# Kernel optimization log

Measured on AMD Instinct MI355X. Metric: run time of the kernel, lower is better.

## Reference

```python
import jax, jax.numpy as jnp
import numpy as np

N, D, E = 50000, 128, 800000
BN_EPS = 1e-5


def _gcn(x, W, b, row, col, val):
    # dropout with p=0.0 is identity; h = x @ W; out = adj @ h + b (COO SpMM)
    h = x @ W                                    # [N, d]
    msg = val[:, None] * h[col]                  # [E, d] gather + scale
    agg = jax.ops.segment_sum(msg, row, num_segments=x.shape[0])  # scatter-add
    return agg + b


def _predictor(x, W1, b1, gamma, beta, a, W2, b2):
    h = x @ W1 + b1
    mu = jnp.mean(h, axis=0)
    var = jnp.mean((h - mu) ** 2, axis=0)        # biased var (torch BN train mode)
    hn = (h - mu) / jnp.sqrt(var + BN_EPS) * gamma + beta
    hp = jnp.where(hn >= 0, hn, a * hn)          # PReLU, single shared alpha
    return hp @ W2 + b2


def _byol_loss(p, t):
    pn = p / jnp.linalg.norm(p, axis=-1, keepdims=True)
    tn = t / jnp.linalg.norm(t, axis=-1, keepdims=True)
    return 2.0 - 2.0 * jnp.sum(pn * tn, axis=-1)


def setup_inputs() -> dict:
    key = jax.random.key(0)
    ks = jax.random.split(key, 16)
    xavier = float(np.sqrt(6.0 / (D + D)))
    x = jax.random.normal(ks[0], (N, D), dtype=jnp.float32)
    perb = 0.05 * jax.random.normal(ks[1], (N, D), dtype=jnp.float32)
    edge_row = jax.random.randint(ks[2], (E,), 0, N, dtype=jnp.int32)
    edge_col = jax.random.randint(ks[3], (E,), 0, N, dtype=jnp.int32)
    edge_val = jax.random.uniform(ks[4], (E,), dtype=jnp.float32)
    W = jax.random.uniform(ks[5], (D, D), minval=-xavier, maxval=xavier, dtype=jnp.float32)
    b = jnp.zeros((D,), dtype=jnp.float32)
    # target encoder is a deepcopy at init; give it its own values to test the math
    Wt = jax.random.uniform(ks[6], (D, D), minval=-xavier, maxval=xavier, dtype=jnp.float32)
    bt = jnp.zeros((D,), dtype=jnp.float32)
    lin = float(1.0 / np.sqrt(D))
    W1 = jax.random.uniform(ks[7], (D, D), minval=-lin, maxval=lin, dtype=jnp.float32)
    b1 = jax.random.uniform(ks[8], (D,), minval=-lin, maxval=lin, dtype=jnp.float32)
    bn_gamma = jnp.ones((D,), dtype=jnp.float32)
    bn_beta = jnp.zeros((D,), dtype=jnp.float32)
    prelu_a = jnp.asarray(0.25, dtype=jnp.float32)
    W2 = jax.random.uniform(ks[9], (D, D), minval=-lin, maxval=lin, dtype=jnp.float32)
    b2 = jax.random.uniform(ks[10], (D,), minval=-lin, maxval=lin, dtype=jnp.float32)
    return dict(x=x, perb=perb, edge_row=edge_row, edge_col=edge_col, edge_val=edge_val,
                W=W, b=b, Wt=Wt, bt=bt, W1=W1, b1=b1, bn_gamma=bn_gamma,
                bn_beta=bn_beta, prelu_a=prelu_a, W2=W2, b2=b2)


def reference(x, perb, edge_row, edge_col, edge_val, W, b, Wt, bt,
              W1, b1, bn_gamma, bn_beta, prelu_a, W2, b2):
    x1 = x
    x2 = x + perb
    enc_x2 = _gcn(x2, W, b, edge_row, edge_col, edge_val)
    embed = x2 + enc_x2
    online_x = _gcn(x1, W, b, edge_row, edge_col, edge_val)
    online_y = enc_x2
    target_y = jax.lax.stop_gradient(_gcn(x1, Wt, bt, edge_row, edge_col, edge_val))
    target_x = jax.lax.stop_gradient(_gcn(x2, Wt, bt, edge_row, edge_col, edge_val))
    px = _predictor(online_x, W1, b1, bn_gamma, bn_beta, prelu_a, W2, b2)
    py = _predictor(online_y, W1, b1, bn_gamma, bn_beta, prelu_a, W2, b2)
    loss = jnp.mean(_byol_loss(px, target_x) + _byol_loss(py, target_y))
    return embed, loss
```

## Files before the change

kernel.cpp:

```cpp
#include <hip/hip_runtime.h>
#include <hip/hip_fp16.h>
#include <stdint.h>

typedef unsigned short u16;
typedef unsigned int u32;
typedef __attribute__((ext_vector_type(8))) short bf16x8;
typedef __attribute__((ext_vector_type(4))) short bf16x4;
typedef __attribute__((ext_vector_type(4))) float f32x4;

#define DD 128
#define CAP 64
#define STRA 136
#define STRCF 132

__device__ __forceinline__ float bflo(u32 u){ return __uint_as_float(u<<16); }
__device__ __forceinline__ float bfhi(u32 u){ return __uint_as_float(u & 0xffff0000u); }
__device__ __forceinline__ float bf2f(u16 u){ return __uint_as_float(((u32)u)<<16); }
__device__ __forceinline__ u16 f2bf(float f){
  u32 u = __float_as_uint(f);
  return (u16)((u + 0x7fffu + ((u>>16)&1u)) >> 16);
}

#define FMA8(g, vv) do { \
    acc[0] += (vv)*bflo((g).x); acc[1] += (vv)*bfhi((g).x); \
    acc[2] += (vv)*bflo((g).y); acc[3] += (vv)*bfhi((g).y); \
    acc[4] += (vv)*bflo((g).z); acc[5] += (vv)*bfhi((g).z); \
    acc[6] += (vv)*bflo((g).w); acc[7] += (vv)*bfhi((g).w); } while(0)

__global__ __launch_bounds__(256) void kU_init(
    const float* __restrict__ x, const float* __restrict__ perb,
    const float* __restrict__ W, const float* __restrict__ Wt,
    const float* __restrict__ W1, const float* __restrict__ W2,
    u16* __restrict__ T, u16* __restrict__ Bswz,
    u16* __restrict__ W1swz, u16* __restrict__ W2swz,
    int* __restrict__ deg, float* __restrict__ stats,
    float* __restrict__ gbuf, int N)
{
  int f = blockIdx.x*256 + threadIdx.x;
  if (f < N) deg[f] = 0;
  if (f < 512) stats[f] = 0.f;
  if (f < 64) gbuf[f] = 0.f;
  if (f < 65536) {
    int idx = f;
    if (idx < 32768) {
      int j = idx & 7, lane = (idx>>3)&63, nt = (idx>>9)&15, kt = idx>>13;
      int k = kt*32 + (lane>>4)*8 + j, n = nt*16 + (lane&15);
      float v = (n < DD) ? W[k*DD + n] : Wt[k*DD + (n-DD)];
      Bswz[idx] = f2bf(v);
    } else {
      int t = idx - 32768;
      int which = t >> 14; t &= 16383;
      int j = t & 7, lane = (t>>3)&63, nt = (t>>9)&7, kt = (t>>12)&3;
      int k = kt*32 + (lane>>4)*8 + j, n = nt*16 + (lane&15);
      const float* __restrict__ src = which ? W2 : W1;
      u16* __restrict__ dst = which ? W2swz : W1swz;
      dst[t] = f2bf(src[k*DD + n]);
    }
  }
  if (f < N*32) {
    int r = f >> 5, c8 = f & 31;
    const float* src = (c8 < 16) ? (x + (size_t)r*DD + c8*8)
                                 : (perb + (size_t)r*DD + (c8-16)*8);
    float4 a = *(const float4*)src;
    float4 bq = *(const float4*)(src + 4);
    bf16x8 o;
    o[0]=(short)f2bf(a.x); o[1]=(short)f2bf(a.y); o[2]=(short)f2bf(a.z); o[3]=(short)f2bf(a.w);
    o[4]=(short)f2bf(bq.x); o[5]=(short)f2bf(bq.y); o[6]=(short)f2bf(bq.z); o[7]=(short)f2bf(bq.w);
    *(bf16x8*)(T + (size_t)r*256 + c8*8) = o;
  }
}

__global__ __launch_bounds__(256) void k2_bucket(
    const int* __restrict__ row, const int* __restrict__ col,
    const float* __restrict__ val, int E, int* __restrict__ deg,
    u32* __restrict__ perm, int* __restrict__ ovfc, int* __restrict__ ovf)
{
  int e = blockIdx.x*256 + threadIdx.x;
  if (e >= E) return;
  int r = row[e];
  int slot = atomicAdd(&deg[r], 1);
  if (slot < CAP) {
    u32 pk = (u32)(col[e] & 0xffff)
           | ((u32)__half_as_ushort(__float2half(val[e])) << 16);
    perm[(size_t)r*CAP + slot] = pk;
  }
  else { int oi = atomicAdd(ovfc, 1); if (oi < 4096) ovf[oi] = e; }
}

__global__ __launch_bounds__(256) void k3_spmm(
    const u32* __restrict__ perm, const int* __restrict__ deg,
    const u16* __restrict__ T, u16* __restrict__ T2, int N)
{
  int row = blockIdx.x*4 + (threadIdx.x >> 6);
  int l = threadIdx.x & 63;
  if (row >= N) return;
  int dg = deg[row];
  dg = dg < 0 ? 0 : (dg > CAP ? CAP : dg);
  const int half = l >> 5, hl = l & 31;
  const int eoff = hl * 8;
  float acc[8] = {0.f,0.f,0.f,0.f,0.f,0.f,0.f,0.f};
  for (int base = 0; base < dg; base += 64) {
    u32 pk = 0;
    if (base + l < dg) pk = perm[(size_t)row*CAP + base + l];
    int mm = dg - base; if (mm > 64) mm = 64;
    int kmax = (mm + 1) & ~1;
    int j = 0;
    for (; j + 8 <= kmax; j += 8) {
      u32 p0 = (u32)__shfl((int)pk, j + half);
      u32 p1 = (u32)__shfl((int)pk, j + 2 + half);
      u32 p2 = (u32)__shfl((int)pk, j + 4 + half);
      u32 p3 = (u32)__shfl((int)pk, j + 6 + half);
      int c0 = p0 & 0xffff; c0 = (c0 < N) ? c0 : 0;
      int c1 = p1 & 0xffff; c1 = (c1 < N) ? c1 : 0;
      int c2 = p2 & 0xffff; c2 = (c2 < N) ? c2 : 0;
      int c3 = p3 & 0xffff; c3 = (c3 < N) ? c3 : 0;
      float v0 = __half2float(__ushort_as_half((u16)(p0 >> 16)));
      float v1 = __half2float(__ushort_as_half((u16)(p1 >> 16)));
      float v2 = __half2float(__ushort_as_half((u16)(p2 >> 16)));
      float v3 = __half2float(__ushort_as_half((u16)(p3 >> 16)));
      uint4 g0 = *(const uint4*)(T + (size_t)c0*256 + eoff);
      uint4 g1 = *(const uint4*)(T + (size_t)c1*256 + eoff);
      uint4 g2 = *(const uint4*)(T + (size_t)c2*256 + eoff);
      uint4 g3 = *(const uint4*)(T + (size_t)c3*256 + eoff);
      FMA8(g0, v0); FMA8(g1, v1); FMA8(g2, v2); FMA8(g3, v3);
    }
    for (; j < kmax; j += 2) {
      u32 p0 = (u32)__shfl((int)pk, j + half);
      int c0 = p0 & 0xffff; c0 = (c0 < N) ? c0 : 0;
      float v0 = __half2float(__ushort_as_half((u16)(p0 >> 16)));
      uint4 g0 = *(const uint4*)(T + (size_t)c0*256 + eoff);
      FMA8(g0, v0);
    }
  }
  #pragma unroll
  for (int i = 0; i < 8; ++i) acc[i] += __shfl_xor(acc[i], 32);
  int sel = (hl >= 16) ? (hl - 16) : hl;
  bf16x8 ob;
  #pragma unroll
  for (int i = 0; i < 8; ++i) {
    float xv = __shfl(acc[i], sel);
    float o = (hl < 16) ? acc[i] : (xv + acc[i]);
    ob[i] = (short)f2bf(o);
  }
  if (half == 0)
    *(bf16x8*)(T2 + (size_t)row*256 + hl*8) = ob;
}

__global__ __launch_bounds__(256) void k3b_ovf(
    const int* __restrict__ rowI, const int* __restrict__ colI,
    const float* __restrict__ val, const int* __restrict__ ovfc,
    const int* __restrict__ ovf, const u16* __restrict__ T,
    u16* __restrict__ T2)
{
  int n = *ovfc; if (n > 4096) n = 4096;
  for (int i = 0; i < n; ++i) {
    int e = ovf[i];
    int r = rowI[e], c = colI[e];
    float v = val[e];
    int d = threadIdx.x;
    int dl = d & 127;
    float add = v * bf2f(T[(size_t)c*256 + dl]);
    if (d >= 128) add += v * bf2f(T[(size_t)c*256 + 128 + dl]);
    u16* p = &T2[(size_t)r*256 + d];
    *p = f2bf(bf2f(*p) + add);
  }
}

__global__ __launch_bounds__(256, 4) void k4_gemm(
    const u16* __restrict__ T2, const u16* __restrict__ Bswz,
    const u16* __restrict__ W1swz,
    const float* __restrict__ b, const float* __restrict__ bt,
    const float* __restrict__ b1, const u16* __restrict__ T,
    u16* __restrict__ AGGb, float* __restrict__ outE,
    u16* __restrict__ Px, u16* __restrict__ Py,
    float* __restrict__ partial, int N, int NB)
{
  __shared__ __align__(16) u16 As1[64*STRA];
  __shared__ __align__(16) u16 Ct[64*STRA];
  const int tid = threadIdx.x;
  const int r0 = blockIdx.x * 32;
  #pragma unroll
  for (int i = 0; i < 4; ++i) {
    int f = tid + 256*i;
    int row = f >> 4, c8 = f & 15;
    int r = r0 + (row & 31);
    bf16x8 ch = {0,0,0,0,0,0,0,0};
    if (r < N) ch = *(const bf16x8*)(T2 + (size_t)r*256 + (row>>5)*128 + c8*8);
    *(bf16x8*)&As1[row*STRA + c8*8] = ch;
  }
  __syncthreads();
  const int w = tid >> 6, l = tid & 63;
  const int m = l & 15, q = l >> 4;
  const int arow = w*16 + m;
  f32x4 acc[8];
  #pragma unroll
  for (int nt = 0; nt < 8; ++nt) acc[nt] = (f32x4){0.f,0.f,0.f,0.f};
  #pragma unroll
  for (int kt = 0; kt < 4; ++kt) {
    bf16x8 af = *(const bf16x8*)&As1[arow*STRA + kt*32 + q*8];
    #pragma unroll
    for (int nt = 0; nt < 8; ++nt) {
      bf16x8 bfr = *(const bf16x8*)(Bswz + ((size_t)(kt*16 + 8 + nt)*64 + l)*8);
      acc[nt] = __builtin_amdgcn_mfma_f32_16x16x32_bf16(af, bfr, acc[nt], 0, 0, 0);
    }
  }
  #pragma unroll
  for (int nt = 0; nt < 8; ++nt) {
    float bv = bt[nt*16 + m];
    #pragma unroll
    for (int i = 0; i < 4; ++i)
      Ct[(w*16 + q*4 + i)*STRA + nt*16 + m] = f2bf(acc[nt][i] + bv);
  }
  __syncthreads();
  {
    const int ar = tid >> 2, p = tid & 3;
    const int src = r0 + (ar & 31);
    if (src < N) {
      u16* dp = AGGb + (size_t)src*256 + (ar>>5)*128 + p*32;
      const u16* sp = &Ct[ar*STRA + p*32];
      #pragma unroll
      for (int i = 0; i < 4; ++i)
        *(bf16x8*)(dp + i*8) = *(const bf16x8*)(sp + i*8);
    }
  }
  __syncthreads();
  #pragma unroll
  for (int nt = 0; nt < 8; ++nt) acc[nt] = (f32x4){0.f,0.f,0.f,0.f};
  #pragma unroll
  for (int kt = 0; kt < 4; ++kt) {
    bf16x8 af = *(const bf16x8*)&As1[arow*STRA + kt*32 + q*8];
    #pragma unroll
    for (int nt = 0; nt < 8; ++nt) {
      bf16x8 bfr = *(const bf16x8*)(Bswz + ((size_t)(kt*16 + nt)*64 + l)*8);
      acc[nt] = __builtin_amdgcn_mfma_f32_16x16x32_bf16(af, bfr, acc[nt], 0, 0, 0);
    }
  }
  #pragma unroll
  for (int nt = 0; nt < 8; ++nt) {
    float bv = b[nt*16 + m];
    #pragma unroll
    for (int i = 0; i < 4; ++i)
      Ct[(w*16 + q*4 + i)*STRA + nt*16 + m] = f2bf(acc[nt][i] + bv);
  }
  __syncthreads();
  #pragma unroll
  for (int i = 0; i < 2; ++i) {
    int f = tid + 256*i;
    int rr = f >> 4, c8 = f & 15;
    int src = r0 + rr;
    if (src < N) {
      const u16* cp = &Ct[(32+rr)*STRA + c8*8];
      bf16x8 xv = *(const bf16x8*)(T + (size_t)src*256 + c8*8);
      bf16x8 pv = *(const bf16x8*)(T + (size_t)src*256 + 128 + c8*8);
      bf16x8 cv = *(const bf16x8*)cp;
      float4 e0, e1;
      e0.x = bf2f((u16)xv[0])+bf2f((u16)pv[0])+bf2f((u16)cv[0]);
      e0.y = bf2f((u16)xv[1])+bf2f((u16)pv[1])+bf2f((u16)cv[1]);
      e0.z = bf2f((u16)xv[2])+bf2f((u16)pv[2])+bf2f((u16)cv[2]);
      e0.w = bf2f((u16)xv[3])+bf2f((u16)pv[3])+bf2f((u16)cv[3]);
      e1.x = bf2f((u16)xv[4])+bf2f((u16)pv[4])+bf2f((u16)cv[4]);
      e1.y = bf2f((u16)xv[5])+bf2f((u16)pv[5])+bf2f((u16)cv[5]);
      e1.z = bf2f((u16)xv[6])+bf2f((u16)pv[6])+bf2f((u16)cv[6]);
      e1.w = bf2f((u16)xv[7])+bf2f((u16)pv[7])+bf2f((u16)cv[7]);
      float* er = outE + (size_t)src*DD + c8*8;
      *(float4*)er = e0;
      *(float4*)(er+4) = e1;
    }
  }
  #pragma unroll
  for (int nt = 0; nt < 8; ++nt) acc[nt] = (f32x4){0.f,0.f,0.f,0.f};
  #pragma unroll
  for (int kt = 0; kt < 4; ++kt) {
    bf16x8 af = *(const bf16x8*)&Ct[arow*STRA + kt*32 + q*8];
    #pragma unroll
    for (int nt = 0; nt < 8; ++nt) {
      bf16x8 bfr = *(const bf16x8*)(W1swz + ((size_t)(kt*8+nt)*64 + l)*8);
      acc[nt] = __builtin_amdgcn_mfma_f32_16x16x32_bf16(af, bfr, acc[nt], 0, 0, 0);
    }
  }
  float* red = (float*)As1;
  #pragma unroll
  for (int nt = 0; nt < 8; ++nt) {
    float bv = b1[nt*16 + m];
    float sum = 0.f, sq = 0.f;
    #pragma unroll
    for (int i = 0; i < 4; ++i) {
      int src = r0 + ((w*16 + q*4 + i) & 31);
      if (src < N) acc[nt][i] += bv; else acc[nt][i] = 0.f;
      sum += acc[nt][i]; sq += acc[nt][i]*acc[nt][i];
    }
    sum += __shfl_xor(sum, 16); sum += __shfl_xor(sum, 32);
    sq  += __shfl_xor(sq, 16);  sq  += __shfl_xor(sq, 32);
    if (l < 16) {
      red[      w*128 + nt*16 + l] = sum;
      red[512 + w*128 + nt*16 + l] = sq;
    }
  }
  __syncthreads();
  {
    int type = tid >> 7, col = tid & 127;
    float v0 = red[type*512 +   0 + col] + red[type*512 + 128 + col];
    float v1 = red[type*512 + 256 + col] + red[type*512 + 384 + col];
    partial[((size_t)0*NB + blockIdx.x)*256 + tid] = v0;
    partial[((size_t)1*NB + blockIdx.x)*256 + tid] = v1;
  }
  #pragma unroll
  for (int nt = 0; nt < 8; ++nt)
    #pragma unroll
    for (int i = 0; i < 4; ++i)
      Ct[(w*16 + q*4 + i)*STRA + nt*16 + m] = f2bf(acc[nt][i]);
  __syncthreads();
  {
    const int ar = tid >> 2, p = tid & 3;
    const int src = r0 + (ar & 31);
    if (src < N) {
      const u16* sp = &Ct[ar*STRA + p*32];
      u16* dp = ((ar >> 5) ? Py : Px) + (size_t)src*DD + p*32;
      #pragma unroll
      for (int i = 0; i < 4; ++i)
        *(bf16x8*)(dp + i*8) = *(const bf16x8*)(sp + i*8);
    }
  }
}

__global__ __launch_bounds__(256) void k5b_stats(
    const float* __restrict__ partial, float* __restrict__ stats, int nb)
{
  int seg = blockIdx.y, chunk = blockIdx.x, t = threadIdx.x;
  int per = (nb + gridDim.x - 1) / gridDim.x;
  int lo = chunk*per, hi = lo+per; if (hi > nb) hi = nb;
  float s = 0.f;
  const float* p = partial + (size_t)seg*nb*256;
  for (int i = lo; i < hi; ++i) s += p[(size_t)i*256 + t];
  atomicAdd(&stats[seg*256 + t], s);
}

__global__ __launch_bounds__(256) void k6_gemm_loss(
    const u16* __restrict__ Px, const u16* __restrict__ Py,
    const u16* __restrict__ AGGb, const float* __restrict__ stats,
    const float* __restrict__ gamma, const float* __restrict__ beta,
    const float* __restrict__ aP, const u16* __restrict__ W2swz,
    const float* __restrict__ b2, float* __restrict__ gloss, int N)
{
  __shared__ __align__(16) float Cs[64*STRCF];
  u16* As = (u16*)Cs;
  __shared__ float s1s[128], s2s[128];
  __shared__ float gred[4];
  const int tid = threadIdx.x;
  const int seg = blockIdx.y;
  const u16* __restrict__ P = seg ? Py : Px;
  const int toff = seg ? 0 : 128;
  const float invN = 1.f / (float)N;
  if (tid < 128) {
    float mu = stats[seg*256 + tid] * invN;
    float var = stats[seg*256 + 128 + tid] * invN - mu*mu;
    float rstd = rsqrtf(var + 1e-5f);
    float s1 = rstd * gamma[tid];
    s1s[tid] = s1;
    s2s[tid] = beta[tid] - mu*s1;
  }
  const float alpha = aP[0];
  const int r0 = blockIdx.x * 64;
  __syncthreads();
  #pragma unroll
  for (int i = 0; i < 4; ++i) {
    int f = tid + 256*i;
    int row = f >> 4, c8 = f & 15;
    int r = r0 + row;
    bf16x8 ch = {0,0,0,0,0,0,0,0};
    if (r < N) ch = *(const bf16x8*)(P + (size_t)r*DD + c8*8);
    bf16x8 a;
    #pragma unroll
    for (int t2 = 0; t2 < 8; ++t2) {
      int colc = c8*8 + t2;
      float hv = bf2f((u16)ch[t2]);
      float hn = hv*s1s[colc] + s2s[colc];
      hn = hn >= 0.f ? hn : alpha*hn;
      a[t2] = (short)f2bf(hn);
    }
    *(bf16x8*)&As[row*STRA + c8*8] = a;
  }
  __syncthreads();
  const int w = tid >> 6, l = tid & 63;
  const int m = l & 15, q = l >> 4;
  f32x4 acc[8];
  #pragma unroll
  for (int nt = 0; nt < 8; ++nt) acc[nt] = (f32x4){0.f,0.f,0.f,0.f};
  const int arow = w*16 + m;
  #pragma unroll
  for (int kt = 0; kt < 4; ++kt) {
    bf16x8 af = *(const bf16x8*)&As[arow*STRA + kt*32 + q*8];
    #pragma unroll
    for (int nt = 0; nt < 8; ++nt) {
      bf16x8 bfr = *(const bf16x8*)(W2swz + ((size_t)(kt*8+nt)*64 + l)*8);
      acc[nt] = __builtin_amdgcn_mfma_f32_16x16x32_bf16(af, bfr, acc[nt], 0, 0, 0);
    }
  }
  __syncthreads();
  #pragma unroll
  for (int nt = 0; nt < 8; ++nt) {
    float bv = b2[nt*16 + m];
    #pragma unroll
    for (int i = 0; i < 4; ++i)
      Cs[(w*16 + q*4 + i)*STRCF + nt*16 + m] = acc[nt][i] + bv;
  }
  __syncthreads();
  {
    const int rt = tid >> 2, qq = tid & 3;
    const int r = r0 + rt;
    float pp = 0.f, tt = 0.f, pt = 0.f;
    if (r < N) {
      const float* prow = &Cs[rt*STRCF + qq*32];
      const u16* trow = AGGb + (size_t)r*256 + toff + qq*32;
      #pragma unroll
      for (int i = 0; i < 4; ++i) {
        float4 pa = *(const float4*)(prow + i*8);
        float4 pb = *(const float4*)(prow + i*8 + 4);
        uint4 twv = *(const uint4*)(trow + i*8);
        float t0=bflo(twv.x), t1=bfhi(twv.x), t2=bflo(twv.y), t3=bfhi(twv.y);
        float t4=bflo(twv.z), t5=bfhi(twv.z), t6=bflo(twv.w), t7=bfhi(twv.w);
        pp += pa.x*pa.x + pa.y*pa.y + pa.z*pa.z + pa.w*pa.w
            + pb.x*pb.x + pb.y*pb.y + pb.z*pb.z + pb.w*pb.w;
        tt += t0*t0 + t1*t1 + t2*t2 + t3*t3 + t4*t4 + t5*t5 + t6*t6 + t7*t7;
        pt += pa.x*t0 + pa.y*t1 + pa.z*t2 + pa.w*t3
            + pb.x*t4 + pb.y*t5 + pb.z*t6 + pb.w*t7;
      }
    }
    pp += __shfl_xor(pp, 1); pp += __shfl_xor(pp, 2);
    tt += __shfl_xor(tt, 1); tt += __shfl_xor(tt, 2);
    pt += __shfl_xor(pt, 1); pt += __shfl_xor(pt, 2);
    float lsum = (r < N) ? (2.f - 2.f * pt * rsqrtf(pp * tt)) : 0.f;
    lsum += __shfl_xor(lsum, 4);  lsum += __shfl_xor(lsum, 8);
    lsum += __shfl_xor(lsum, 16); lsum += __shfl_xor(lsum, 32);
    if (l == 0) gred[w] = lsum;
  }
  __syncthreads();
  if (tid == 0) atomicAdd(gloss, gred[0]+gred[1]+gred[2]+gred[3]);
}

__global__ void k7_loss(const float* __restrict__ gloss, float* __restrict__ out, int N, int total)
{
  out[total] = gloss[0] / (float)N;
}

extern "C" void kernel_launch(void* const* d_in, const int* in_sizes, int n_in,
                              void* d_out, int out_size, void* d_ws, size_t ws_size,
                              hipStream_t stream)
{
  const float* x    = (const float*)d_in[0];
  const float* perb = (const float*)d_in[1];
  const int*   erow = (const int*)d_in[2];
  const int*   ecol = (const int*)d_in[3];
  const float* eval_= (const float*)d_in[4];
  const float* W    = (const float*)d_in[5];
  const float* b    = (const float*)d_in[6];
  const float* Wt   = (const float*)d_in[7];
  const float* bt   = (const float*)d_in[8];
  const float* W1   = (const float*)d_in[9];
  const float* b1   = (const float*)d_in[10];
  const float* gam  = (const float*)d_in[11];
  const float* bet  = (const float*)d_in[12];
  const float* aP   = (const float*)d_in[13];
  const float* W2   = (const float*)d_in[14];
  const float* b2   = (const float*)d_in[15];
  const int N = in_sizes[0] / DD;
  const int E = in_sizes[2];
  const int NB4 = (N + 31)/32;
  const int NB5 = (N + 63)/64;

  char* ws = (char*)d_ws;
  size_t off = 0;
  auto alloc = [&](size_t bytes) -> void* {
    void* p = ws + off;
    off += (bytes + 255) & ~(size_t)255;
    return p;
  };
  u16*   AGGb = (u16*)  alloc((size_t)N*256*sizeof(u16));
  u16*   T    = (u16*)  alloc((size_t)N*256*sizeof(u16));
  u16*   T2   = (u16*)  alloc((size_t)N*256*sizeof(u16));
  u16*   Px   = (u16*)  alloc((size_t)N*DD*sizeof(u16));
  u16*   Py   = (u16*)  alloc((size_t)N*DD*sizeof(u16));
  int*   deg  = (int*)  alloc((size_t)N*sizeof(int));
  float* stats= (float*)alloc(512*sizeof(float));
  float* gloss= (float*)alloc(256);
  int*   ovfc = (int*)((char*)gloss + 64);
  u32*   perm = (u32*)  alloc((size_t)N*CAP*sizeof(u32));
  int*   ovf  = (int*)  alloc(4096*sizeof(int));
  u16*   Bswz = (u16*)  alloc(32768*sizeof(u16));
  u16*   W1swz= (u16*)  alloc(16384*sizeof(u16));
  u16*   W2swz= (u16*)  alloc(16384*sizeof(u16));
  float* partial = (float*)alloc((size_t)2*NB4*256*sizeof(float));
  if (ws_size < off) return;

  kU_init<<<(N*32 + 255)/256, 256, 0, stream>>>(x, perb, W, Wt, W1, W2,
                                                T, Bswz, W1swz, W2swz,
                                                deg, stats, gloss, N);
  k2_bucket<<<(E + 255)/256, 256, 0, stream>>>(erow, ecol, eval_, E, deg, perm, ovfc, ovf);
  k3_spmm<<<(N + 3)/4, 256, 0, stream>>>(perm, deg, T, T2, N);
  k3b_ovf<<<1, 256, 0, stream>>>(erow, ecol, eval_, ovfc, ovf, T, T2);
  k4_gemm<<<NB4, 256, 0, stream>>>(T2, Bswz, W1swz, b, bt, b1, T,
                                   AGGb, (float*)d_out, Px, Py, partial, N, NB4);
  k5b_stats<<<dim3(16, 2), 256, 0, stream>>>(partial, stats, NB4);
  k6_gemm_loss<<<dim3(NB5, 2), 256, 0, stream>>>(Px, Py, AGGb, stats, gam, bet, aP,
                                                 W2swz, b2, gloss, N);
  k7_loss<<<1, 1, 0, stream>>>(gloss, (float*)d_out, N, N*DD);
}
```

Measured before the change: 332.5 us.

## Quantize perturbation to int8 and pack node features into 12-byte groups

The gathered feature table now stores x as bf16 and perb as int8 scaled by 256, packed into 384 bytes per node instead of 512. The SpMM gather reads 12 bytes per lane and rebuilds x2 = x + perb on the fly, so each half-wave writes its own output half directly. This cuts the bytes moved by the random gather that dominates SpMM. In exchange, perb is quantized with step 1/256 and clamped at about ±0.5, which adds error to the embed output and to the x2 path, and the packed layout gives less aligned 12-byte loads.

```diff
diff --git a/kernel.cpp b/kernel.cpp
--- a/kernel.cpp
+++ b/kernel.cpp
@@ -4,6 +4,7 @@
 
 typedef unsigned short u16;
 typedef unsigned int u32;
+typedef unsigned char u8;
 typedef __attribute__((ext_vector_type(8))) short bf16x8;
 typedef __attribute__((ext_vector_type(4))) short bf16x4;
 typedef __attribute__((ext_vector_type(4))) float f32x4;
@@ -12,6 +13,8 @@
 #define CAP 64
 #define STRA 136
 #define STRCF 132
+#define PSC 256.f
+#define IPSC (1.f/256.f)
 
 __device__ __forceinline__ float bflo(u32 u){ return __uint_as_float(u<<16); }
 __device__ __forceinline__ float bfhi(u32 u){ return __uint_as_float(u & 0xffff0000u); }
@@ -21,17 +24,20 @@
   return (u16)((u + 0x7fffu + ((u>>16)&1u)) >> 16);
 }
 
-#define FMA8(g, vv) do { \
-    acc[0] += (vv)*bflo((g).x); acc[1] += (vv)*bfhi((g).x); \
-    acc[2] += (vv)*bflo((g).y); acc[3] += (vv)*bfhi((g).y); \
-    acc[4] += (vv)*bflo((g).z); acc[5] += (vv)*bfhi((g).z); \
-    acc[6] += (vv)*bflo((g).w); acc[7] += (vv)*bfhi((g).w); } while(0)
+#define FMAXP(g, vv, vqv) do { \
+    ax[0] += (vv)*bflo((g).x); ax[1] += (vv)*bfhi((g).x); \
+    ax[2] += (vv)*bflo((g).y); ax[3] += (vv)*bfhi((g).y); \
+    int d_ = (int)(g).z; \
+    ap[0] += (vqv)*(float)(signed char)(d_); \
+    ap[1] += (vqv)*(float)(signed char)(d_>>8); \
+    ap[2] += (vqv)*(float)(signed char)(d_>>16); \
+    ap[3] += (vqv)*(float)(d_>>24); } while(0)
 
 __global__ __launch_bounds__(256) void kU_init(
     const float* __restrict__ x, const float* __restrict__ perb,
     const float* __restrict__ W, const float* __restrict__ Wt,
     const float* __restrict__ W1, const float* __restrict__ W2,
-    u16* __restrict__ T, u16* __restrict__ Bswz,
+    u8* __restrict__ Tg, u16* __restrict__ Bswz,
     u16* __restrict__ W1swz, u16* __restrict__ W2swz,
     int* __restrict__ deg, float* __restrict__ stats,
     float* __restrict__ gbuf, int N)
@@ -58,15 +64,19 @@
     }
   }
   if (f < N*32) {
-    int r = f >> 5, c8 = f & 31;
-    const float* src = (c8 < 16) ? (x + (size_t)r*DD + c8*8)
-                                 : (perb + (size_t)r*DD + (c8-16)*8);
-    float4 a = *(const float4*)src;
-    float4 bq = *(const float4*)(src + 4);
-    bf16x8 o;
-    o[0]=(short)f2bf(a.x); o[1]=(short)f2bf(a.y); o[2]=(short)f2bf(a.z); o[3]=(short)f2bf(a.w);
-    o[4]=(short)f2bf(bq.x); o[5]=(short)f2bf(bq.y); o[6]=(short)f2bf(bq.z); o[7]=(short)f2bf(bq.w);
-    *(bf16x8*)(T + (size_t)r*256 + c8*8) = o;
+    int r = f >> 5, hl = f & 31;
+    float4 xa = *(const float4*)(x    + (size_t)r*DD + hl*4);
+    float4 pa = *(const float4*)(perb + (size_t)r*DD + hl*4);
+    u32 d0 = (u32)f2bf(xa.x) | ((u32)f2bf(xa.y) << 16);
+    u32 d1 = (u32)f2bf(xa.z) | ((u32)f2bf(xa.w) << 16);
+    int q0 = (int)rintf(pa.x*PSC); q0 = q0 < -127 ? -127 : (q0 > 127 ? 127 : q0);
+    int q1 = (int)rintf(pa.y*PSC); q1 = q1 < -127 ? -127 : (q1 > 127 ? 127 : q1);
+    int q2 = (int)rintf(pa.z*PSC); q2 = q2 < -127 ? -127 : (q2 > 127 ? 127 : q2);
+    int q3 = (int)rintf(pa.w*PSC); q3 = q3 < -127 ? -127 : (q3 > 127 ? 127 : q3);
+    u32 d2 = (u32)(q0 & 0xff) | ((u32)(q1 & 0xff) << 8)
+           | ((u32)(q2 & 0xff) << 16) | ((u32)(q3 & 0xff) << 24);
+    uint3 o; o.x = d0; o.y = d1; o.z = d2;
+    *(uint3*)(Tg + (size_t)r*384 + hl*12) = o;
   }
 }
 
@@ -89,7 +99,7 @@
 
 __global__ __launch_bounds__(256) void k3_spmm(
     const u32* __restrict__ perm, const int* __restrict__ deg,
-    const u16* __restrict__ T, u16* __restrict__ T2, int N)
+    const u8* __restrict__ Tg, u16* __restrict__ T2, int N)
 {
   int row = blockIdx.x*4 + (threadIdx.x >> 6);
   int l = threadIdx.x & 63;
@@ -97,8 +107,9 @@
   int dg = deg[row];
   dg = dg < 0 ? 0 : (dg > CAP ? CAP : dg);
   const int half = l >> 5, hl = l & 31;
-  const int eoff = hl * 8;
-  float acc[8] = {0.f,0.f,0.f,0.f,0.f,0.f,0.f,0.f};
+  const int loff = hl * 12;
+  float ax[4] = {0.f,0.f,0.f,0.f};
+  float ap[4] = {0.f,0.f,0.f,0.f};
   for (int base = 0; base < dg; base += 64) {
     u32 pk = 0;
     if (base + l < dg) pk = perm[(size_t)row*CAP + base + l];
@@ -118,38 +129,41 @@
       float v1 = __half2float(__ushort_as_half((u16)(p1 >> 16)));
       float v2 = __half2float(__ushort_as_half((u16)(p2 >> 16)));
       float v3 = __half2float(__ushort_as_half((u16)(p3 >> 16)));
-      uint4 g0 = *(const uint4*)(T + (size_t)c0*256 + eoff);
-      uint4 g1 = *(const uint4*)(T + (size_t)c1*256 + eoff);
-      uint4 g2 = *(const uint4*)(T + (size_t)c2*256 + eoff);
-      uint4 g3 = *(const uint4*)(T + (size_t)c3*256 + eoff);
-      FMA8(g0, v0); FMA8(g1, v1); FMA8(g2, v2); FMA8(g3, v3);
+      uint3 g0 = *(const uint3*)(Tg + (size_t)c0*384 + loff);
+      uint3 g1 = *(const uint3*)(Tg + (size_t)c1*384 + loff);
+      uint3 g2 = *(const uint3*)(Tg + (size_t)c2*384 + loff);
+      uint3 g3 = *(const uint3*)(Tg + (size_t)c3*384 + loff);
+      float vq0 = v0*IPSC, vq1 = v1*IPSC, vq2 = v2*IPSC, vq3 = v3*IPSC;
+      FMAXP(g0, v0, vq0); FMAXP(g1, v1, vq1);
+      FMAXP(g2, v2, vq2); FMAXP(g3, v3, vq3);
     }
     for (; j < kmax; j += 2) {
       u32 p0 = (u32)__shfl((int)pk, j + half);
       int c0 = p0 & 0xffff; c0 = (c0 < N) ? c0 : 0;
       float v0 = __half2float(__ushort_as_half((u16)(p0 >> 16)));
-      uint4 g0 = *(const uint4*)(T + (size_t)c0*256 + eoff);
-      FMA8(g0, v0);
-    }
-  }
-  #pragma unroll
-  for (int i = 0; i < 8; ++i) acc[i] += __shfl_xor(acc[i], 32);
-  int sel = (hl >= 16) ? (hl - 16) : hl;
-  bf16x8 ob;
-  #pragma unroll
-  for (int i = 0; i < 8; ++i) {
-    float xv = __shfl(acc[i], sel);
-    float o = (hl < 16) ? acc[i] : (xv + acc[i]);
+      uint3 g0 = *(const uint3*)(Tg + (size_t)c0*384 + loff);
+      float vq0 = v0*IPSC;
+      FMAXP(g0, v0, vq0);
+    }
+  }
+  #pragma unroll
+  for (int i = 0; i < 4; ++i) {
+    ax[i] += __shfl_xor(ax[i], 32);
+    ap[i] += __shfl_xor(ap[i], 32);
+  }
+  bf16x4 ob;
+  #pragma unroll
+  for (int i = 0; i < 4; ++i) {
+    float o = half ? (ax[i] + ap[i]) : ax[i];
     ob[i] = (short)f2bf(o);
   }
-  if (half == 0)
-    *(bf16x8*)(T2 + (size_t)row*256 + hl*8) = ob;
+  *(bf16x4*)(T2 + (size_t)row*256 + half*128 + hl*4) = ob;
 }
 
 __global__ __launch_bounds__(256) void k3b_ovf(
     const int* __restrict__ rowI, const int* __restrict__ colI,
     const float* __restrict__ val, const int* __restrict__ ovfc,
-    const int* __restrict__ ovf, const u16* __restrict__ T,
+    const int* __restrict__ ovf, const u8* __restrict__ Tg,
     u16* __restrict__ T2)
 {
   int n = *ovfc; if (n > 4096) n = 4096;
@@ -159,8 +173,13 @@
     float v = val[e];
     int d = threadIdx.x;
     int dl = d & 127;
-    float add = v * bf2f(T[(size_t)c*256 + dl]);
-    if (d >= 128) add += v * bf2f(T[(size_t)c*256 + 128 + dl]);
+    const u8* tgc = Tg + (size_t)c*384 + (dl>>2)*12;
+    float xv = bf2f(*(const u16*)(tgc + (dl&3)*2));
+    float add = v * xv;
+    if (d >= 128) {
+      int qb = (int)(signed char)tgc[8 + (dl&3)];
+      add = v * (xv + (float)qb * IPSC);
+    }
     u16* p = &T2[(size_t)r*256 + d];
     *p = f2bf(bf2f(*p) + add);
   }
@@ -170,7 +189,7 @@
     const u16* __restrict__ T2, const u16* __restrict__ Bswz,
     const u16* __restrict__ W1swz,
     const float* __restrict__ b, const float* __restrict__ bt,
-    const float* __restrict__ b1, const u16* __restrict__ T,
+    const float* __restrict__ b1, const u8* __restrict__ Tg,
     u16* __restrict__ AGGb, float* __restrict__ outE,
     u16* __restrict__ Px, u16* __restrict__ Py,
     float* __restrict__ partial, int N, int NB)
@@ -250,18 +269,19 @@
     int src = r0 + rr;
     if (src < N) {
       const u16* cp = &Ct[(32+rr)*STRA + c8*8];
-      bf16x8 xv = *(const bf16x8*)(T + (size_t)src*256 + c8*8);
-      bf16x8 pv = *(const bf16x8*)(T + (size_t)src*256 + 128 + c8*8);
-      bf16x8 cv = *(const bf16x8*)cp;
+      const u8* tg = Tg + (size_t)src*384 + c8*24;
+      uint3 ga = *(const uint3*)tg;
+      uint3 gb = *(const uint3*)(tg + 12);
+      int da = (int)ga.z, db = (int)gb.z;
       float4 e0, e1;
-      e0.x = bf2f((u16)xv[0])+bf2f((u16)pv[0])+bf2f((u16)cv[0]);
-      e0.y = bf2f((u16)xv[1])+bf2f((u16)pv[1])+bf2f((u16)cv[1]);
-      e0.z = bf2f((u16)xv[2])+bf2f((u16)pv[2])+bf2f((u16)cv[2]);
-      e0.w = bf2f((u16)xv[3])+bf2f((u16)pv[3])+bf2f((u16)cv[3]);
-      e1.x = bf2f((u16)xv[4])+bf2f((u16)pv[4])+bf2f((u16)cv[4]);
-      e1.y = bf2f((u16)xv[5])+bf2f((u16)pv[5])+bf2f((u16)cv[5]);
-      e1.z = bf2f((u16)xv[6])+bf2f((u16)pv[6])+bf2f((u16)cv[6]);
-      e1.w = bf2f((u16)xv[7])+bf2f((u16)pv[7])+bf2f((u16)cv[7]);
+      e0.x = bflo(ga.x) + IPSC*(float)(signed char)(da)     + bf2f(cp[0]);
+      e0.y = bfhi(ga.x) + IPSC*(float)(signed char)(da>>8)  + bf2f(cp[1]);
+      e0.z = bflo(ga.y) + IPSC*(float)(signed char)(da>>16) + bf2f(cp[2]);
+      e0.w = bfhi(ga.y) + IPSC*(float)(da>>24)              + bf2f(cp[3]);
+      e1.x = bflo(gb.x) + IPSC*(float)(signed char)(db)     + bf2f(cp[4]);
+      e1.y = bfhi(gb.x) + IPSC*(float)(signed char)(db>>8)  + bf2f(cp[5]);
+      e1.z = bflo(gb.y) + IPSC*(float)(signed char)(db>>16) + bf2f(cp[6]);
+      e1.w = bfhi(gb.y) + IPSC*(float)(db>>24)              + bf2f(cp[7]);
       float* er = outE + (size_t)src*DD + c8*8;
       *(float4*)er = e0;
       *(float4*)(er+4) = e1;
@@ -476,7 +496,7 @@
     return p;
   };
   u16*   AGGb = (u16*)  alloc((size_t)N*256*sizeof(u16));
-  u16*   T    = (u16*)  alloc((size_t)N*256*sizeof(u16));
+  u8*    Tg   = (u8*)   alloc((size_t)N*384);
   u16*   T2   = (u16*)  alloc((size_t)N*256*sizeof(u16));
   u16*   Px   = (u16*)  alloc((size_t)N*DD*sizeof(u16));
   u16*   Py   = (u16*)  alloc((size_t)N*DD*sizeof(u16));
@@ -493,12 +513,12 @@
   if (ws_size < off) return;
 
   kU_init<<<(N*32 + 255)/256, 256, 0, stream>>>(x, perb, W, Wt, W1, W2,
-                                                T, Bswz, W1swz, W2swz,
+                                                Tg, Bswz, W1swz, W2swz,
                                                 deg, stats, gloss, N);
   k2_bucket<<<(E + 255)/256, 256, 0, stream>>>(erow, ecol, eval_, E, deg, perm, ovfc, ovf);
-  k3_spmm<<<(N + 3)/4, 256, 0, stream>>>(perm, deg, T, T2, N);
-  k3b_ovf<<<1, 256, 0, stream>>>(erow, ecol, eval_, ovfc, ovf, T, T2);
-  k4_gemm<<<NB4, 256, 0, stream>>>(T2, Bswz, W1swz, b, bt, b1, T,
+  k3_spmm<<<(N + 3)/4, 256, 0, stream>>>(perm, deg, Tg, T2, N);
+  k3b_ovf<<<1, 256, 0, stream>>>(erow, ecol, eval_, ovfc, ovf, Tg, T2);
+  k4_gemm<<<NB4, 256, 0, stream>>>(T2, Bswz, W1swz, b, bt, b1, Tg,
                                    AGGb, (float*)d_out, Px, Py, partial, N, NB4);
   k5b_stats<<<dim3(16, 2), 256, 0, stream>>>(partial, stats, NB4);
   k6_gemm_loss<<<dim3(NB5, 2), 256, 0, stream>>>(Px, Py, AGGb, stats, gam, bet, aP,
```

Result: faster. 313.8 us (-5.6%).
